# Kernel optimization log

Measured on AMD Instinct MI355X. Metric: run time of the kernel, lower is better.

Reference implementation:

```python
import jax, jax.numpy as jnp
import numpy as np

B, L, A, K = 8, 256, 15, 9
EDGE_SIZE = 16
CA = 1  # BBHeavyAtom.CA index


def setup_inputs() -> dict:
    key = jax.random.key(0)
    k1, k2, k3, k4 = jax.random.split(key, 4)
    pos_heavyatom = jax.random.normal(k1, (B, L, A, 3), jnp.float32) * 3.0
    aa = jax.random.randint(k2, (B, L), 0, 21, jnp.int32)
    atom_types = jax.random.randint(k3, (B, L, A), 0, 38, jnp.int32)
    mask_atoms = jnp.ones((B, L, A), dtype=bool)
    block_lengths = jnp.full((B, L), A, jnp.int32)
    lengths = jnp.full((B,), L, jnp.int32)
    # two segments per sample (e.g. antibody / antigen) so intra+inter edges exist
    fragment_type = jnp.broadcast_to((jnp.arange(L) >= L // 2).astype(jnp.int32), (B, L))
    edge_emb = jax.random.normal(k4, (2, EDGE_SIZE), jnp.float32) * 0.02
    return {"pos_heavyatom": pos_heavyatom, "aa": aa, "atom_types": atom_types,
            "mask_atoms": mask_atoms, "block_lengths": block_lengths,
            "lengths": lengths, "fragment_type": fragment_type, "edge_emb": edge_emb}


def _block_dist(pos, mask_atoms):
    """Min unit-pair distance between every pair of blocks. pos [B,L,A,3] -> [B,L,L]."""
    Xf = pos.reshape(B, L * A, 3)
    x2 = jnp.sum(Xf * Xf, axis=-1)  # [B, N]
    d2 = x2[:, :, None] + x2[:, None, :] - 2.0 * jnp.einsum('bnd,bmd->bnm', Xf, Xf)
    d = jnp.sqrt(jnp.maximum(d2, 0.0))  # [B, N, N]
    # unit is kept iff its atom mask AND its residue's CA mask are set
    mask_res = mask_atoms[:, :, CA]                           # [B, L]
    valid = (mask_atoms & mask_res[:, :, None]).reshape(B, L * A)
    pair_ok = valid[:, :, None] & valid[:, None, :]
    d = jnp.where(pair_ok, d, jnp.inf)
    # scatter_min over block edges == min over the (A, A) unit-pair tiles
    return d.reshape(B, L, A, L, A).min(axis=(2, 4))          # [B, L, L]


def _knn_edges(dist, cand_mask):
    """For each source block (row), pick K nearest candidate dst blocks. Returns [2, B*L*K] global ids."""
    dm = jnp.where(cand_mask, dist, jnp.inf)
    _, idx = jax.lax.top_k(-dm, K)                            # [B, L, K] local dst ids
    src = jnp.broadcast_to(jnp.arange(L, dtype=jnp.int32)[None, :, None], (B, L, K))
    offs = (jnp.arange(B, dtype=jnp.int32) * L)[:, None, None]
    return jnp.stack([(src + offs).reshape(-1), (idx.astype(jnp.int32) + offs).reshape(-1)], axis=0)


def reference(pos_heavyatom, aa, atom_types, mask_atoms, block_lengths, lengths,
              fragment_type, edge_emb):
    # segment ids: fragment_type 2 is merged into segment 1
    seg = jnp.where(fragment_type == 2, 1, fragment_type)     # [B, L]
    dist = _block_dist(pos_heavyatom, mask_atoms)             # [B, L, L]

    same_seg = seg[:, :, None] == seg[:, None, :]
    eye = jnp.eye(L, dtype=bool)[None]
    intra_edges = _knn_edges(dist, same_seg & ~eye)           # same segment, no self-loop
    inter_edges = _knn_edges(dist, ~same_seg)                 # different segment

    edges = jnp.concatenate([intra_edges, inter_edges], axis=1)  # [2, 2*B*L*K]
    edge_type = jnp.concatenate([jnp.zeros(intra_edges.shape[1], jnp.int32),
                                 jnp.ones(inter_edges.shape[1], jnp.int32)])
    edge_attr = edge_emb[edge_type]                           # [2*B*L*K, 16]

    block_id = jnp.arange(B * L * A, dtype=jnp.int32) // A    # global block id per unit
    batch_id = jnp.arange(B * L, dtype=jnp.int32) // L        # batch id per block
    return block_id, batch_id, edges, edge_attr
```

## Files before the change

### kernel.cpp

```cpp
#include <hip/hip_runtime.h>


#define BB   8
#define LL   256
#define AA   15
#define KK   9

#define O_BATCH   30720
#define O_EDGES   32768
#define NE_HALF   18432
#define NE        36864
#define O_ATTR    106496
#define DELTA     0.005f
#define EPS2      2e-3
#define HBASE     1904
#define NBIN      512
#define MAXM      128

__device__ __forceinline__ float rfl(float v) {
    return __int_as_float(__builtin_amdgcn_readfirstlane(__float_as_int(v)));
}

__global__ __launch_bounds__(256) void edge_fused_kernel(
    const float* __restrict__ pos,
    const int*   __restrict__ frag,
    const float* __restrict__ emb,
    float*       __restrict__ out)
{
    const int blk = blockIdx.x;
    const int b   = blk >> 8;
    const int i   = blk & 255;
    const int j   = threadIdx.x;

    __shared__ float4 sAi4[AA];
    __shared__ double dAi[AA * 3];
    __shared__ double dX2i[AA];
    __shared__ int    sHist[2*NBIN];
    __shared__ int    sList[MAXM];
    __shared__ double sVal[MAXM];
    __shared__ int    sRList[MAXM];
    __shared__ int    sCnt, sRCnt;

    if (j < AA)  out[blk * AA + j]  = (float)blk;
    if (j == AA) out[O_BATCH + blk] = (float)b;
    {
        int idx = blk * 288 + j;
        out[O_ATTR + idx] = emb[(((idx >> 4) < NE_HALF) ? 0 : 16) + (idx & 15)];
        if (j < 32) {
            int idx2 = idx + 256;
            out[O_ATTR + idx2] = emb[(((idx2 >> 4) < NE_HALF) ? 0 : 16) + (idx2 & 15)];
        }
    }

    if (j < AA) {
        const float* p = pos + (size_t)blk * 45 + j * 3;
        float x = p[0], y = p[1], z = p[2];
        sAi4[j] = make_float4(-2.0f * x, -2.0f * y, -2.0f * z,
                              x*x + y*y + z*z);
        double dx = (double)x, dy = (double)y, dz = (double)z;
        dAi[3*j] = dx; dAi[3*j+1] = dy; dAi[3*j+2] = dz;
        dX2i[j] = dx*dx + dy*dy + dz*dz;
    }
    #pragma unroll
    for (int q = 0; q < 4; ++q) sHist[j + (q << 8)] = 0;
    if (j == 255) sCnt = 0;
    if (j == 254) sRCnt = 0;

    const int ftj  = frag[b * LL + j];
    const int segj = (ftj == 2) ? 1 : ftj;
    const int fti  = frag[blk];
    const int segi = (fti == 2) ? 1 : fti;
    const int cls  = (j == i) ? -1 : ((segj == segi) ? 0 : 1);
    __syncthreads();

    float Ax[AA], Ay[AA], Az[AA], Aw[AA];
    #pragma unroll
    for (int a = 0; a < AA; ++a) {
        float4 A = sAi4[a];
        Ax[a] = rfl(A.x); Ay[a] = rfl(A.y);
        Az[a] = rfl(A.z); Aw[a] = rfl(A.w);
    }

    const float* pj = pos + (size_t)(b * LL + j) * 45;
    float d32 = INFINITY;
    #pragma unroll 1
    for (int cb = 0; cb < AA; cb += 5) {
        float cx[5], cy[5], cz[5], c2[5], m[5];
        #pragma unroll
        for (int q = 0; q < 5; ++q) {
            cx[q] = pj[3*(cb+q) + 0];
            cy[q] = pj[3*(cb+q) + 1];
            cz[q] = pj[3*(cb+q) + 2];
            c2[q] = cx[q]*cx[q] + cy[q]*cy[q] + cz[q]*cz[q];
            m[q]  = INFINITY;
        }
        #pragma unroll
        for (int a = 0; a < AA; ++a) {
            #pragma unroll
            for (int q = 0; q < 5; ++q) {
                float dp = fmaf(Ax[a], cx[q], fmaf(Ay[a], cy[q],
                            fmaf(Az[a], cz[q], Aw[a])));
                m[q] = fminf(m[q], dp);
            }
        }
        #pragma unroll
        for (int q = 0; q < 5; ++q)
            d32 = fminf(d32, m[q] + c2[q]);
    }
    d32 = fmaxf(d32, 0.0f);

    if (cls >= 0) {
        int bin = (int)(__float_as_uint(d32) >> 19) - HBASE;
        bin = min(NBIN - 1, max(0, bin));
        atomicAdd(&sHist[cls * NBIN + bin], 1);
    }
    __syncthreads();

    const int lane = j & 63;
    float T[2];
    #pragma unroll
    for (int cw = 0; cw < 2; ++cw) {
        int c[8], s = 0;
        #pragma unroll
        for (int q = 0; q < 8; ++q) {
            c[q] = sHist[cw * NBIN + 8*lane + q];
            s += c[q];
        }
        int cum = s;
        #pragma unroll
        for (int off = 1; off < 64; off <<= 1) {
            int v = __shfl_up(cum, off, 64);
            if (lane >= off) cum += v;
        }
        unsigned long long msk = __ballot(cum >= KK);
        float t_ = INFINITY;
        if (msk != 0ull) {
            int f = __builtin_ctzll(msk);
            if (lane == f) {
                int before = cum - s, bin = -1;
                #pragma unroll
                for (int q = 0; q < 8; ++q) {
                    before += c[q];
                    if (bin < 0 && before >= KK) bin = 8*f + q;
                }
                t_ = (bin >= NBIN - 1) ? INFINITY
                   : __uint_as_float((unsigned)(HBASE + bin + 1) << 19);
            }
            t_ = __shfl(t_, f, 64);
        }
        T[cw] = t_;
    }

    if (cls >= 0 && d32 <= T[cls] + DELTA) {
        int p = atomicAdd(&sCnt, 1);
        if (p < MAXM) {
            sList[p] = (j << 1) | cls;
            sVal[p]  = (double)d32;
        }
    }
    __syncthreads();
    const int cnt = min(sCnt, MAXM);

    if (j < cnt) {
        double my = sVal[j];
        int mycls = sList[j] & 1;
        bool need = false;
        for (int u = 0; u < cnt; ++u) {
            if (u != j && (sList[u] & 1) == mycls &&
                fabs(sVal[u] - my) <= EPS2) need = true;
        }
        if (need) { int p = atomicAdd(&sRCnt, 1); sRList[p] = j; }
    }
    __syncthreads();

    {
        const int rcnt = sRCnt;
        const int wv = j >> 6;
        for (int base = 0; base < rcnt; base += 4) {
            int t = base + wv;
            double dmin = INFINITY;
            int slot = -1;
            if (t < rcnt) {
                slot = sRList[t];
                int cand = sList[slot] >> 1;
                const float* pc = pos + (size_t)(b * LL + cand) * 45;
                for (int p = lane; p < 225; p += 64) {
                    int a = p / 15, c = p - a * 15;
                    double cx = (double)pc[3*c], cy = (double)pc[3*c+1],
                           cz = (double)pc[3*c+2];
                    double dot = dAi[3*a]*cx + dAi[3*a+1]*cy + dAi[3*a+2]*cz;
                    double d2  = (dX2i[a] + (cx*cx + cy*cy + cz*cz))
                               - 2.0 * dot;
                    dmin = fmin(dmin, d2);
                }
            }
            #pragma unroll
            for (int off = 1; off < 64; off <<= 1)
                dmin = fmin(dmin, __shfl_xor(dmin, off, 64));
            if (lane == 0 && t < rcnt) sVal[slot] = fmax(dmin, 0.0);
        }
    }
    __syncthreads();

    if (j < cnt) {
        int e   = sList[j];
        int cnd = e >> 1, mycls = e & 1;
        double key = sVal[j];
        int r = 0;
        for (int u = 0; u < cnt; ++u) {
            int eu = sList[u];
            if ((eu & 1) == mycls) {
                double ku = sVal[u];
                int cu = eu >> 1;
                if (ku < key || (ku == key && cu < cnd)) ++r;
            }
        }
        r -= (mycls == 0 && r > 0 && false) ? 0 : 0;
        if (r < KK) {
            int eo = (mycls == 0 ? 0 : NE_HALF) + blk * KK + r;
            out[O_EDGES + eo]      = (float)blk;
            out[O_EDGES + NE + eo] = (float)(b * LL + cnd);
        }
    }
}

extern "C" void kernel_launch(void* const* d_in, const int* in_sizes, int n_in,
                              void* d_out, int out_size, void* d_ws, size_t ws_size,
                              hipStream_t stream) {
    const float* pos  = (const float*)d_in[0];
    const int*   frag = (const int*)d_in[6];
    const float* emb  = (const float*)d_in[7];
    float* out = (float*)d_out;

    edge_fused_kernel<<<dim3(BB * LL), dim3(256), 0, stream>>>(pos, frag, emb, out);
}
```

Baseline: 99.48 us.

## Split block-distance computation into symmetric tiled kernel before selection

Moves the block-pair minimum distance computation into a separate kernel that handles 16x16 upper-triangle tiles through shared memory. Each tile is written to a workspace matrix in both orientations, so symmetry halves the arithmetic and the j-side atom data is reused across 16 rows. The selection kernel now reads one distance per thread instead of recomputing it, and the histogram is coarsened to 128 bins. The cost is an extra launch, a global round-trip of the distance matrix, and coarser bins that may let more candidates through the threshold.

```diff
diff --git a/kernel.cpp b/kernel.cpp
--- a/kernel.cpp
+++ b/kernel.cpp
@@ -13,16 +13,79 @@
 #define O_ATTR    106496
 #define DELTA     0.005f
 #define EPS2      2e-3
-#define HBASE     1904
-#define NBIN      512
+#define HBASE     448
+#define NBIN      128
 #define MAXM      128
 
-__device__ __forceinline__ float rfl(float v) {
-    return __int_as_float(__builtin_amdgcn_readfirstlane(__float_as_int(v)));
+#define TW        16
+#define NTILE     136
+
+__global__ __launch_bounds__(256) void dist_kernel(
+    const float* __restrict__ pos,
+    float*       __restrict__ D)
+{
+    const int bx = blockIdx.x;
+    const int b  = bx / NTILE;
+    const int t  = bx - b * NTILE;
+    int ti = (int)((33.0f - sqrtf(1089.0f - 8.0f * (float)t)) * 0.5f);
+    while (ti * (33 - ti) / 2 > t) --ti;
+    while ((ti + 1) * (32 - ti) / 2 <= t) ++ti;
+    const int tj = ti + (t - ti * (33 - ti) / 2);
+    const int I0 = ti * TW, J0 = tj * TW;
+
+    __shared__ float4 sI[AA][TW];
+    __shared__ float4 sJ[AA][TW];
+
+    const int tid = threadIdx.x;
+    if (tid < 240) {
+        const int bl = tid / AA, a = tid - bl * AA;
+        {
+            const float* p = pos + ((size_t)(b * LL + I0 + bl) * 45) + a * 3;
+            float x = p[0], y = p[1], z = p[2];
+            sI[a][bl] = make_float4(-2.f*x, -2.f*y, -2.f*z, x*x + y*y + z*z);
+        }
+        {
+            const float* p = pos + ((size_t)(b * LL + J0 + bl) * 45) + a * 3;
+            float x = p[0], y = p[1], z = p[2];
+            sJ[a][bl] = make_float4(x, y, z, x*x + y*y + z*z);
+        }
+    }
+    __syncthreads();
+
+    const int il = tid >> 4, jl = tid & 15;
+
+    float4 J[AA];
+    float  m[AA];
+    #pragma unroll
+    for (int c = 0; c < AA; ++c) { J[c] = sJ[c][jl]; m[c] = INFINITY; }
+
+    #pragma unroll
+    for (int a = 0; a < AA; ++a) {
+        float4 A = sI[a][il];
+        #pragma unroll
+        for (int c = 0; c < AA; ++c) {
+            float dp = fmaf(A.x, J[c].x,
+                       fmaf(A.y, J[c].y,
+                       fmaf(A.z, J[c].z, A.w)));
+            m[c] = fminf(m[c], dp);
+        }
+    }
+    float v = INFINITY;
+    #pragma unroll
+    for (int c = 0; c < AA; ++c) v = fminf(v, m[c] + J[c].w);
+    v = fmaxf(v, 0.0f);
+
+    if (ti != tj || jl >= il) {
+        const int i = I0 + il, j = J0 + jl;
+        const size_t base = ((size_t)b) << 16;
+        D[base + (i << 8) + j] = v;
+        D[base + (j << 8) + i] = v;
+    }
 }
 
-__global__ __launch_bounds__(256) void edge_fused_kernel(
+__global__ __launch_bounds__(256) void select_kernel(
     const float* __restrict__ pos,
+    const float* __restrict__ D,
     const int*   __restrict__ frag,
     const float* __restrict__ emb,
     float*       __restrict__ out)
@@ -32,10 +95,9 @@
     const int i   = blk & 255;
     const int j   = threadIdx.x;
 
-    __shared__ float4 sAi4[AA];
     __shared__ double dAi[AA * 3];
     __shared__ double dX2i[AA];
-    __shared__ int    sHist[2*NBIN];
+    __shared__ int    sHist[2 * NBIN];
     __shared__ int    sList[MAXM];
     __shared__ double sVal[MAXM];
     __shared__ int    sRList[MAXM];
@@ -54,15 +116,11 @@
 
     if (j < AA) {
         const float* p = pos + (size_t)blk * 45 + j * 3;
-        float x = p[0], y = p[1], z = p[2];
-        sAi4[j] = make_float4(-2.0f * x, -2.0f * y, -2.0f * z,
-                              x*x + y*y + z*z);
-        double dx = (double)x, dy = (double)y, dz = (double)z;
+        double dx = (double)p[0], dy = (double)p[1], dz = (double)p[2];
         dAi[3*j] = dx; dAi[3*j+1] = dy; dAi[3*j+2] = dz;
         dX2i[j] = dx*dx + dy*dy + dz*dz;
     }
-    #pragma unroll
-    for (int q = 0; q < 4; ++q) sHist[j + (q << 8)] = 0;
+    if (j < 2 * NBIN) sHist[j] = 0;
     if (j == 255) sCnt = 0;
     if (j == 254) sRCnt = 0;
 
@@ -71,46 +129,12 @@
     const int fti  = frag[blk];
     const int segi = (fti == 2) ? 1 : fti;
     const int cls  = (j == i) ? -1 : ((segj == segi) ? 0 : 1);
-    __syncthreads();
-
-    float Ax[AA], Ay[AA], Az[AA], Aw[AA];
-    #pragma unroll
-    for (int a = 0; a < AA; ++a) {
-        float4 A = sAi4[a];
-        Ax[a] = rfl(A.x); Ay[a] = rfl(A.y);
-        Az[a] = rfl(A.z); Aw[a] = rfl(A.w);
-    }
-
-    const float* pj = pos + (size_t)(b * LL + j) * 45;
-    float d32 = INFINITY;
-    #pragma unroll 1
-    for (int cb = 0; cb < AA; cb += 5) {
-        float cx[5], cy[5], cz[5], c2[5], m[5];
-        #pragma unroll
-        for (int q = 0; q < 5; ++q) {
-            cx[q] = pj[3*(cb+q) + 0];
-            cy[q] = pj[3*(cb+q) + 1];
-            cz[q] = pj[3*(cb+q) + 2];
-            c2[q] = cx[q]*cx[q] + cy[q]*cy[q] + cz[q]*cz[q];
-            m[q]  = INFINITY;
-        }
-        #pragma unroll
-        for (int a = 0; a < AA; ++a) {
-            #pragma unroll
-            for (int q = 0; q < 5; ++q) {
-                float dp = fmaf(Ax[a], cx[q], fmaf(Ay[a], cy[q],
-                            fmaf(Az[a], cz[q], Aw[a])));
-                m[q] = fminf(m[q], dp);
-            }
-        }
-        #pragma unroll
-        for (int q = 0; q < 5; ++q)
-            d32 = fminf(d32, m[q] + c2[q]);
-    }
-    d32 = fmaxf(d32, 0.0f);
+
+    const float d32 = D[(((size_t)b) << 16) + (i << 8) + j];
+    __syncthreads();
 
     if (cls >= 0) {
-        int bin = (int)(__float_as_uint(d32) >> 19) - HBASE;
+        int bin = (int)(__float_as_uint(d32) >> 21) - HBASE;
         bin = min(NBIN - 1, max(0, bin));
         atomicAdd(&sHist[cls * NBIN + bin], 1);
     }
@@ -120,12 +144,9 @@
     float T[2];
     #pragma unroll
     for (int cw = 0; cw < 2; ++cw) {
-        int c[8], s = 0;
-        #pragma unroll
-        for (int q = 0; q < 8; ++q) {
-            c[q] = sHist[cw * NBIN + 8*lane + q];
-            s += c[q];
-        }
+        int c0 = sHist[cw * NBIN + 2*lane];
+        int c1 = sHist[cw * NBIN + 2*lane + 1];
+        int s  = c0 + c1;
         int cum = s;
         #pragma unroll
         for (int off = 1; off < 64; off <<= 1) {
@@ -137,14 +158,10 @@
         if (msk != 0ull) {
             int f = __builtin_ctzll(msk);
             if (lane == f) {
-                int before = cum - s, bin = -1;
-                #pragma unroll
-                for (int q = 0; q < 8; ++q) {
-                    before += c[q];
-                    if (bin < 0 && before >= KK) bin = 8*f + q;
-                }
+                int before = cum - s;
+                int bin = (before + c0 >= KK) ? 2*f : 2*f + 1;
                 t_ = (bin >= NBIN - 1) ? INFINITY
-                   : __uint_as_float((unsigned)(HBASE + bin + 1) << 19);
+                   : __uint_as_float((unsigned)(HBASE + bin + 1) << 21);
             }
             t_ = __shfl(t_, f, 64);
         }
@@ -215,7 +232,6 @@
                 if (ku < key || (ku == key && cu < cnd)) ++r;
             }
         }
-        r -= (mycls == 0 && r > 0 && false) ? 0 : 0;
         if (r < KK) {
             int eo = (mycls == 0 ? 0 : NE_HALF) + blk * KK + r;
             out[O_EDGES + eo]      = (float)blk;
@@ -231,6 +247,9 @@
     const int*   frag = (const int*)d_in[6];
     const float* emb  = (const float*)d_in[7];
     float* out = (float*)d_out;
-
-    edge_fused_kernel<<<dim3(BB * LL), dim3(256), 0, stream>>>(pos, frag, emb, out);
+    float* Dm  = (float*)d_ws;
+
+    dist_kernel<<<dim3(BB * NTILE), dim3(256), 0, stream>>>(pos, Dm);
+    select_kernel<<<dim3(BB * LL), dim3(256), 0, stream>>>(pos, Dm, frag,
+                                                           emb, out);
 }
```

Result: faster. 89.60 us (median of 2 runs) (-9.9%).
